# Performance work log

Hardware: AMD Instinct MI355X
Metric: run time of the kernel (lower is better)

## Reference

```python
import jax, jax.numpy as jnp
import numpy as np

B, S, D = 2, 2048, 2048
H = 16
HD = D // H  # 128
ROPE_BASE = 10000.0


def _rope_cos_sin(seq_len, head_dim):
    inv_freq = 1.0 / (ROPE_BASE ** (jnp.arange(0, head_dim, 2, dtype=jnp.float32) / head_dim))
    t = jnp.arange(seq_len, dtype=jnp.float32)
    freqs = jnp.einsum('i,j->ij', t, inv_freq)  # [S, HD/2]
    emb = jnp.concatenate([freqs, freqs], axis=-1)  # [S, HD]
    return jnp.cos(emb)[None, None], jnp.sin(emb)[None, None]  # [1,1,S,HD]


def _rotate_half(x):
    x1, x2 = jnp.split(x, 2, axis=-1)
    return jnp.concatenate([-x2, x1], axis=-1)


def setup_inputs() -> dict:
    key = jax.random.key(0)
    k1, k2, k3 = jax.random.split(key, 3)
    hidden_states = jax.random.normal(k1, (B, S, D), dtype=jnp.float32)
    w_qkv = jax.random.normal(k2, (D, 3 * D), dtype=jnp.float32) * (D ** -0.5)
    w_o = jax.random.normal(k3, (D, D), dtype=jnp.float32) * (D ** -0.5)
    return {"hidden_states": hidden_states, "w_qkv": w_qkv, "w_o": w_o}


def reference(hidden_states, w_qkv, w_o):
    b, s, _ = hidden_states.shape
    qkv = jnp.einsum('bsd,de->bse', hidden_states, w_qkv)  # [B,S,3D]
    q, k, v = jnp.split(qkv, 3, axis=-1)
    # [B,H,S,HD]
    q = q.reshape(b, s, H, HD).transpose(0, 2, 1, 3)
    k = k.reshape(b, s, H, HD).transpose(0, 2, 1, 3)
    v = v.reshape(b, s, H, HD).transpose(0, 2, 1, 3)
    cos, sin = _rope_cos_sin(s, HD)
    q = q * cos + _rotate_half(q) * sin
    k = k * cos + _rotate_half(k) * sin
    scale = 1.0 / np.sqrt(HD).astype(np.float32)
    scores = jnp.einsum('bhqd,bhkd->bhqk', q, k) * scale  # [B,H,S,S]
    causal = jnp.triu(jnp.ones((s, s), dtype=bool), k=1)
    scores = jnp.where(causal, -jnp.inf, scores)
    attn = jax.nn.softmax(scores, axis=-1)
    out = jnp.einsum('bhqk,bhkd->bhqd', attn, v)  # [B,H,S,HD]
    out = out.transpose(0, 2, 1, 3).reshape(b, s, H * HD)
    return jnp.einsum('bsd,de->bse', out, w_o)
```

## Files before the change

### kernel.cpp

```cpp
#include <hip/hip_runtime.h>
#include <math.h>

typedef unsigned short u16;
typedef short s16x8 __attribute__((ext_vector_type(8)));
typedef float f32x4 __attribute__((ext_vector_type(4)));

#define ATTN_SCALE 0.08838834764831845f
#define ATTN_SC2 0.1275174245f
#define NEG_BIG -1.0e30f

__device__ __forceinline__ u16 f2bf(float f) {
  union { float f; unsigned u; } c; c.f = f;
  return (u16)((c.u + 0x7fffu + ((c.u >> 16) & 1u)) >> 16);
}
__device__ __forceinline__ float bf2f(u16 v) {
  union { unsigned u; float f; } c; c.u = ((unsigned)v) << 16;
  return c.f;
}
__device__ __forceinline__ f32x4 mfma16(s16x8 a, s16x8 b, f32x4 c) {
  return __builtin_amdgcn_mfma_f32_16x16x32_bf16(a, b, c, 0, 0, 0);
}
__device__ __forceinline__ void gl_lds16(const u16* g, u16* l) {
  __builtin_amdgcn_global_load_lds(
      (const __attribute__((address_space(1))) unsigned int*)g,
      (__attribute__((address_space(3))) unsigned int*)l, 16, 0, 0);
}

__global__ __launch_bounds__(256) void k_cast(const float* __restrict__ in,
                                              u16* __restrict__ out, int n4) {
  const int i = blockIdx.x * 256 + threadIdx.x;
  if (i >= n4) return;
  const float4 v = ((const float4*)in)[i];
  ushort4 o;
  o.x = f2bf(v.x); o.y = f2bf(v.y); o.z = f2bf(v.z); o.w = f2bf(v.w);
  ((ushort4*)out)[i] = o;
}

__global__ __launch_bounds__(256) void k_transpose_cast(const float* __restrict__ in,
                                                        u16* __restrict__ out,
                                                        int R, int C) {
  __shared__ __attribute__((aligned(16))) u16 tile[32][33];
  const int c0 = blockIdx.x * 32, r0 = blockIdx.y * 32;
  const int tx = threadIdx.x, ty = threadIdx.y;
#pragma unroll
  for (int i = 0; i < 4; ++i)
    tile[ty + 8 * i][tx] = f2bf(in[(r0 + ty + 8 * i) * C + c0 + tx]);
  __syncthreads();
#pragma unroll
  for (int i = 0; i < 4; ++i)
    out[(c0 + ty + 8 * i) * R + r0 + tx] = tile[tx][ty + 8 * i];
}

__global__ __launch_bounds__(256) void k_vtrans(const u16* __restrict__ qkv,
                                                u16* __restrict__ vt) {
  __shared__ __attribute__((aligned(16))) u16 tile[32][33];
  const int bh = blockIdx.z, b = bh >> 4, h = bh & 15;
  const int s0 = blockIdx.x * 32, d0 = blockIdx.y * 32;
  const int tx = threadIdx.x, ty = threadIdx.y;
#pragma unroll
  for (int i = 0; i < 4; ++i) {
    const int s = s0 + ty + 8 * i;
    tile[ty + 8 * i][tx] = qkv[(b * 2048 + s) * 6144 + 4096 + h * 128 + d0 + tx];
  }
  __syncthreads();
#pragma unroll
  for (int i = 0; i < 4; ++i) {
    const int d = d0 + ty + 8 * i;
    vt[bh * 262144 + d * 2048 + s0 + tx] = tile[tx][ty + 8 * i];
  }
}

__global__ __launch_bounds__(256) void k_rope(u16* __restrict__ qkv) {
  const int id = blockIdx.x * 256 + threadIdx.x;
  const int j = id & 63;
  const int h = (id >> 6) & 15;
  const int sec = (id >> 10) & 1;
  const int m = id >> 11;
  const int s = m & 2047;
  const int base = m * 6144 + sec * 2048 + h * 128 + j;
  const float q0 = bf2f(qkv[base]);
  const float q1 = bf2f(qkv[base + 64]);
  const float inv = exp2f((float)j * -0.20762050593046014f);
  const float ang = (float)s * inv;
  float c, sn;
  sincosf(ang, &sn, &c);
  qkv[base]      = f2bf(q0 * c - q1 * sn);
  qkv[base + 64] = f2bf(q1 * c + q0 * sn);
}

template <bool A_F32, typename OUT_T>
__global__ __launch_bounds__(256) void k_gemm_lds(const void* __restrict__ Ap, int lda,
                                                  const u16* __restrict__ BT,
                                                  OUT_T* __restrict__ C, int ldc,
                                                  int K) {
  __shared__ __attribute__((aligned(16))) u16 As[128 * 32];
  __shared__ __attribute__((aligned(16))) u16 Bs[128 * 32];
  const int tid = threadIdx.x;
  const int lane = tid & 63, wave = tid >> 6;
  const int lm = lane & 15, quad = lane >> 4;
  const int wm = wave >> 1, wn = wave & 1;
  const int m0 = blockIdx.y * 128, n0 = blockIdx.x * 128;
  const int srow = lane >> 2, scol = (lane & 3) * 8;

  const f32x4 fzero = {0.f, 0.f, 0.f, 0.f};
  f32x4 acc[4][4];
#pragma unroll
  for (int i = 0; i < 4; ++i)
#pragma unroll
    for (int j = 0; j < 4; ++j) acc[i][j] = fzero;

  for (int k0 = 0; k0 < K; k0 += 32) {
    __syncthreads();
    if constexpr (A_F32) {
      const float* Af = (const float*)Ap;
#pragma unroll
      for (int i = 0; i < 2; ++i) {
        const int seg = tid + 256 * i;
        const int row = seg >> 2, c8 = (seg & 3) * 8;
        const float4 u = *(const float4*)&Af[(m0 + row) * lda + k0 + c8];
        const float4 w = *(const float4*)&Af[(m0 + row) * lda + k0 + c8 + 4];
        uint4 pk;
        pk.x = (unsigned)f2bf(u.x) | ((unsigned)f2bf(u.y) << 16);
        pk.y = (unsigned)f2bf(u.z) | ((unsigned)f2bf(u.w) << 16);
        pk.z = (unsigned)f2bf(w.x) | ((unsigned)f2bf(w.y) << 16);
        pk.w = (unsigned)f2bf(w.z) | ((unsigned)f2bf(w.w) << 16);
        *(uint4*)&As[row * 32 + c8] = pk;
      }
#pragma unroll
      for (int j = 0; j < 2; ++j) {
        const int rb = wave * 32 + j * 16;
        gl_lds16(&BT[(n0 + rb + srow) * K + k0 + scol], &Bs[rb * 32]);
      }
    } else {
      const u16* Ab = (const u16*)Ap;
#pragma unroll
      for (int j = 0; j < 2; ++j) {
        const int rb = wave * 32 + j * 16;
        gl_lds16(&Ab[(m0 + rb + srow) * lda + k0 + scol], &As[rb * 32]);
        gl_lds16(&BT[(n0 + rb + srow) * K + k0 + scol], &Bs[rb * 32]);
      }
    }
    __syncthreads();

    s16x8 af[4], bfr[4];
#pragma unroll
    for (int t = 0; t < 4; ++t) {
      af[t]  = *(const s16x8*)&As[(wm * 64 + t * 16 + lm) * 32 + quad * 8];
      bfr[t] = *(const s16x8*)&Bs[(wn * 64 + t * 16 + lm) * 32 + quad * 8];
    }
#pragma unroll
    for (int mt = 0; mt < 4; ++mt)
#pragma unroll
      for (int nt = 0; nt < 4; ++nt)
        acc[mt][nt] = mfma16(af[mt], bfr[nt], acc[mt][nt]);
  }
#pragma unroll
  for (int mt = 0; mt < 4; ++mt)
#pragma unroll
    for (int nt = 0; nt < 4; ++nt)
#pragma unroll
      for (int r = 0; r < 4; ++r) {
        const float v = acc[mt][nt][r];
        const int idx = (m0 + wm * 64 + mt * 16 + quad * 4 + r) * ldc +
                        n0 + wn * 64 + nt * 16 + lm;
        if constexpr (sizeof(OUT_T) == 2) C[idx] = f2bf(v);
        else                              C[idx] = v;
      }
}

template <typename OUT_T>
__global__ __launch_bounds__(512, 2) void k_gemm256(const u16* __restrict__ A, int lda,
                                                    const u16* __restrict__ BT, int ldb,
                                                    OUT_T* __restrict__ C, int ldc) {
  __shared__ __attribute__((aligned(16))) u16 As[3][2][256 * 32];
  __shared__ __attribute__((aligned(16))) u16 Bs[3][2][128 * 32];
  const int tid = threadIdx.x;
  const int lane = tid & 63, wave = tid >> 6;
  const int lm = lane & 15, quad = lane >> 4;
  const int wm = wave >> 1, wn = wave & 1;

  int bid = (blockIdx.x & 7) * (gridDim.x >> 3) + (blockIdx.x >> 3);
  const int m0 = (bid & 15) * 256;
  const int n0 = (bid >> 4) * 128;

  const int srow = lane >> 2, schunk = (lane & 3) * 8;
  auto stage_h = [&](int t, int h) {
    const int bi = t % 3;
    const int k0 = t * 64 + h * 32 + schunk;
    gl_lds16(&BT[(n0 + wave * 16 + srow) * ldb + k0],
             &Bs[bi][h][(wave * 16) * 32]);
    gl_lds16(&A[(m0 + wave * 32 + srow) * lda + k0],
             &As[bi][h][(wave * 32) * 32]);
    gl_lds16(&A[(m0 + wave * 32 + 16 + srow) * lda + k0],
             &As[bi][h][(wave * 32 + 16) * 32]);
  };

  const f32x4 fzero = {0.f, 0.f, 0.f, 0.f};
  f32x4 acc[4][4];
#pragma unroll
  for (int i = 0; i < 4; ++i)
#pragma unroll
    for (int j = 0; j < 4; ++j) acc[i][j] = fzero;

  stage_h(0, 0); stage_h(0, 1); stage_h(1, 0); stage_h(1, 1);
  asm volatile("s_waitcnt vmcnt(9)" ::: "memory");
  asm volatile("s_barrier" ::: "memory");

  for (int c = 0; c < 32; ++c) {
    const int bi = c % 3;
#pragma unroll
    for (int p = 0; p < 2; ++p) {
      s16x8 bfr[4], afr[4];
#pragma unroll
      for (int nt = 0; nt < 4; ++nt)
        bfr[nt] = *(const s16x8*)
            &Bs[bi][p][(wn * 64 + nt * 16 + lm) * 32 + quad * 8];
#pragma unroll
      for (int i = 0; i < 4; ++i)
        afr[i] = *(const s16x8*)
            &As[bi][p][(wm * 64 + i * 16 + lm) * 32 + quad * 8];
      if (c < 30) stage_h(c + 2, p);
      if (c < 30) {
        asm volatile("s_waitcnt vmcnt(9)" ::: "memory");
      } else if (c == 30) {
        if (p == 0) asm volatile("s_waitcnt vmcnt(6)" ::: "memory");
        else        asm volatile("s_waitcnt vmcnt(3)" ::: "memory");
      } else {
        if (p == 0) asm volatile("s_waitcnt vmcnt(0)" ::: "memory");
      }
      asm volatile("s_barrier" ::: "memory");
      __builtin_amdgcn_s_setprio(1);
#pragma unroll
      for (int i = 0; i < 4; ++i)
#pragma unroll
        for (int nt = 0; nt < 4; ++nt)
          acc[i][nt] = mfma16(afr[i], bfr[nt], acc[i][nt]);
      __builtin_amdgcn_s_setprio(0);
      if (!(c == 31 && p == 1)) asm volatile("s_barrier" ::: "memory");
    }
  }

#pragma unroll
  for (int i = 0; i < 4; ++i)
#pragma unroll
    for (int nt = 0; nt < 4; ++nt)
#pragma unroll
      for (int r = 0; r < 4; ++r) {
        const float v = acc[i][nt][r];
        const int idx = (m0 + wm * 64 + i * 16 + quad * 4 + r) * ldc +
                        n0 + wn * 64 + nt * 16 + lm;
        if constexpr (sizeof(OUT_T) == 2) C[idx] = f2bf(v);
        else                              C[idx] = v;
      }
}

__global__ __launch_bounds__(256) void k_attn(u16* __restrict__ qkv,
                                              const u16* __restrict__ vt) {
  __shared__ __attribute__((aligned(16))) u16 Ks[2][64 * 128];
  __shared__ __attribute__((aligned(16))) u16 Vs[2][128 * 64];
  __shared__ __attribute__((aligned(16))) u16 Ps[4 * 16 * 72];
  const int bh = blockIdx.x, pair = blockIdx.y;
  const int b = bh >> 4, h = bh & 15;
  const int tid = threadIdx.x;
  const int lane = tid & 63, wave = tid >> 6;
  const int lm = lane & 15, quad = lane >> 4;
  const int pbase = wave * 1152;
  const int sw = lm & 7;
  const f32x4 fzero = {0.f, 0.f, 0.f, 0.f};

  const int phase_end = pair;

  auto dma_tile = [&](int kt0, int buf) {
#pragma unroll
    for (int i = 0; i < 4; ++i) {
      const int row = i * 16 + wave * 4 + (lane >> 4);
      const int cc = (lane & 15) ^ (row & 7);
      gl_lds16(&qkv[(b * 2048 + kt0 + row) * 6144 + 2048 + h * 128 + cc * 8],
               &Ks[buf][(i * 16 + wave * 4) * 128]);
    }
#pragma unroll
    for (int i = 0; i < 4; ++i) {
      const int row = i * 32 + wave * 8 + (lane >> 3);
      const int cc = (lane & 7) ^ (row & 7);
      gl_lds16(&vt[bh * 262144 + row * 2048 + kt0 + cc * 8],
               &Vs[buf][(i * 32 + wave * 8) * 64]);
    }
  };

  dma_tile(0, 0);

  int qtile = pair;
  int qb = qtile * 64;
  int qrow = qb + wave * 16 + lm;
  int qoff = (b * 2048 + qrow) * 6144 + h * 128;
  s16x8 qfrag[4];
#pragma unroll
  for (int c = 0; c < 4; ++c)
    qfrag[c] = *(const s16x8*)&qkv[qoff + c * 32 + quad * 8];
  f32x4 o[8];
#pragma unroll
  for (int dt = 0; dt < 8; ++dt) o[dt] = fzero;
  float m_run = NEG_BIG, l_run = 0.f;

  __syncthreads();

  for (int it = 0; it < 33; ++it) {
    const int kt0 = (it <= phase_end ? it : it - phase_end - 1) * 64;
    const int buf = it & 1;

    if (it < 32) {
      const int nkt = (it + 1 <= phase_end ? it + 1 : it - phase_end) * 64;
      dma_tile(nkt, buf ^ 1);
    }

    f32x4 sa[4];
#pragma unroll
    for (int ss = 0; ss < 4; ++ss) sa[ss] = fzero;
#pragma unroll
    for (int ss = 0; ss < 4; ++ss)
#pragma unroll
      for (int c = 0; c < 4; ++c) {
        const int ccs = (c * 4 + quad) ^ sw;
        s16x8 a = *(const s16x8*)&Ks[buf][(ss * 16 + lm) * 128 + ccs * 8];
        sa[ss] = mfma16(a, qfrag[c], sa[ss]);
      }

    float p[4][4];
    float vmax = NEG_BIG;
    if (kt0 + 63 > qrow - lm) {
#pragma unroll
      for (int ss = 0; ss < 4; ++ss)
#pragma unroll
        for (int r = 0; r < 4; ++r) {
          const int kg = kt0 + ss * 16 + quad * 4 + r;
          float v = sa[ss][r] * ATTN_SC2;
          if (kg > qrow) v = NEG_BIG;
          p[ss][r] = v;
          vmax = fmaxf(vmax, v);
        }
    } else {
#pragma unroll
      for (int ss = 0; ss < 4; ++ss)
#pragma unroll
        for (int r = 0; r < 4; ++r) {
          const float v = sa[ss][r] * ATTN_SC2;
          p[ss][r] = v;
          vmax = fmaxf(vmax, v);
        }
    }
    vmax = fmaxf(vmax, __shfl_xor(vmax, 16, 64));
    vmax = fmaxf(vmax, __shfl_xor(vmax, 32, 64));
    if (!__all(vmax <= m_run)) {
      const float m_new = fmaxf(m_run, vmax);
      const float alpha = exp2f(m_run - m_new);
      l_run *= alpha;
#pragma unroll
      for (int dt = 0; dt < 8; ++dt) o[dt] *= alpha;
      m_run = m_new;
    }
    float rsum = 0.f;
#pragma unroll
    for (int ss = 0; ss < 4; ++ss)
#pragma unroll
      for (int r = 0; r < 4; ++r) {
        p[ss][r] = exp2f(p[ss][r] - m_run);
        rsum += p[ss][r];
      }
    rsum += __shfl_xor(rsum, 16, 64);
    rsum += __shfl_xor(rsum, 32, 64);
    l_run += rsum;

#pragma unroll
    for (int ss = 0; ss < 4; ++ss)
#pragma unroll
      for (int rp = 0; rp < 2; ++rp) {
        unsigned pk;
        asm("v_cvt_pk_bf16_f32 %0, %1, %2"
            : "=v"(pk) : "v"(p[ss][rp * 2]), "v"(p[ss][rp * 2 + 1]));
        *(unsigned*)&Ps[pbase + lm * 72 + ss * 16 + quad * 4 + rp * 2] = pk;
      }
    const s16x8 pv0 = *(const s16x8*)&Ps[pbase + lm * 72 + quad * 8];
    const s16x8 pv1 = *(const s16x8*)&Ps[pbase + lm * 72 + 32 + quad * 8];

#pragma unroll
    for (int dt = 0; dt < 8; ++dt) {
      const int c0 = (quad ^ sw) * 8, c1 = ((4 + quad) ^ sw) * 8;
      s16x8 a0 = *(const s16x8*)&Vs[buf][(dt * 16 + lm) * 64 + c0];
      s16x8 a1 = *(const s16x8*)&Vs[buf][(dt * 16 + lm) * 64 + c1];
      o[dt] = mfma16(a1, pv1, mfma16(a0, pv0, o[dt]));
    }

    if (it == phase_end) {
      const float inv_l = 1.0f / l_run;
#pragma unroll
      for (int dt = 0; dt < 8; ++dt)
#pragma unroll
        for (int r = 0; r < 4; ++r)
          qkv[qoff + dt * 16 + quad * 4 + r] = f2bf(o[dt][r] * inv_l);
      qtile = 31 - pair;
      qb = qtile * 64;
      qrow = qb + wave * 16 + lm;
      qoff = (b * 2048 + qrow) * 6144 + h * 128;
#pragma unroll
      for (int c = 0; c < 4; ++c)
        qfrag[c] = *(const s16x8*)&qkv[qoff + c * 32 + quad * 8];
#pragma unroll
      for (int dt = 0; dt < 8; ++dt) o[dt] = fzero;
      m_run = NEG_BIG; l_run = 0.f;
    }

    if (it < 32) __syncthreads();
  }

  const float inv_l = 1.0f / l_run;
#pragma unroll
  for (int dt = 0; dt < 8; ++dt)
#pragma unroll
    for (int r = 0; r < 4; ++r)
      qkv[qoff + dt * 16 + quad * 4 + r] = f2bf(o[dt][r] * inv_l);
}

extern "C" void kernel_launch(void* const* d_in, const int* in_sizes, int n_in,
                              void* d_out, int out_size, void* d_ws, size_t ws_size,
                              hipStream_t stream) {
  const float* hidden = (const float*)d_in[0];
  const float* w_qkv  = (const float*)d_in[1];
  const float* w_o    = (const float*)d_in[2];
  float* out = (float*)d_out;
  u16* ws = (u16*)d_ws;

  u16* qkv   = ws;
  u16* wqkvT = ws + 25165824;
  u16* vt    = ws + 25165824;
  u16* woT   = ws + 33554432;
  u16* hb    = ws + 37748736;
  const bool fast = ws_size >= (size_t)46137344 * 2;

  dim3 tb(32, 8);
  k_transpose_cast<<<dim3(192, 64), tb, 0, stream>>>(w_qkv, wqkvT, 2048, 6144);
  if (fast) {
    k_cast<<<8192, 256, 0, stream>>>(hidden, hb, 2097152);
    k_gemm256<u16><<<768, 512, 0, stream>>>(hb, 2048, wqkvT, 2048, qkv, 6144);
  } else {
    k_gemm_lds<true, u16><<<dim3(48, 32), 256, 0, stream>>>(hidden, 2048, wqkvT,
                                                            qkv, 6144, 2048);
  }
  k_rope<<<32768, 256, 0, stream>>>(qkv);
  k_vtrans<<<dim3(64, 4, 32), tb, 0, stream>>>(qkv, vt);
  k_transpose_cast<<<dim3(64, 64), tb, 0, stream>>>(w_o, woT, 2048, 2048);
  k_attn<<<dim3(32, 16), 256, 0, stream>>>(qkv, vt);
  if (fast) {
    k_gemm256<float><<<256, 512, 0, stream>>>(qkv, 6144, woT, 2048, out, 2048);
  } else {
    k_gemm_lds<false, float><<<dim3(16, 32), 256, 0, stream>>>(qkv, 6144, woT,
                                                               out, 2048, 2048);
  }
}
```

Before: 410.1 us.

## Process two 16-row query groups per wave to reuse K/V fragments

Each wave now handles 32 query rows (two groups of 16) instead of 16, so the block's query tile grows from 64 to 128 rows. K and V fragments are loaded from LDS once per tile and fed to MFMAs for both groups, which halves LDS reads per unit of compute and halves the number of blocks and K/V tile streams. The paired causal schedule is adjusted to 128-row tiles and launch_bounds(256,1) is set. In exchange register pressure rises considerably and the grid shrinks to 256 blocks, which lowers occupancy and parallelism.

After: 432.5 us. 1.05x slower.

```diff
diff --git a/kernel.cpp b/kernel.cpp
--- a/kernel.cpp
+++ b/kernel.cpp
@@ -254,8 +254,8 @@
       }
 }
 
-__global__ __launch_bounds__(256) void k_attn(u16* __restrict__ qkv,
-                                              const u16* __restrict__ vt) {
+__global__ __launch_bounds__(256, 1) void k_attn(u16* __restrict__ qkv,
+                                                 const u16* __restrict__ vt) {
   __shared__ __attribute__((aligned(16))) u16 Ks[2][64 * 128];
   __shared__ __attribute__((aligned(16))) u16 Vs[2][128 * 64];
   __shared__ __attribute__((aligned(16))) u16 Ps[4 * 16 * 72];
@@ -268,7 +268,7 @@
   const int sw = lm & 7;
   const f32x4 fzero = {0.f, 0.f, 0.f, 0.f};
 
-  const int phase_end = pair;
+  const int phase_end = 2 * pair + 1;
 
   auto dma_tile = [&](int kt0, int buf) {
 #pragma unroll
@@ -289,135 +289,164 @@
 
   dma_tile(0, 0);
 
+  int qbase[2], qoff[2];
+  s16x8 qfrag[2][4];
   int qtile = pair;
-  int qb = qtile * 64;
-  int qrow = qb + wave * 16 + lm;
-  int qoff = (b * 2048 + qrow) * 6144 + h * 128;
-  s16x8 qfrag[4];
-#pragma unroll
-  for (int c = 0; c < 4; ++c)
-    qfrag[c] = *(const s16x8*)&qkv[qoff + c * 32 + quad * 8];
-  f32x4 o[8];
-#pragma unroll
-  for (int dt = 0; dt < 8; ++dt) o[dt] = fzero;
-  float m_run = NEG_BIG, l_run = 0.f;
+#pragma unroll
+  for (int g = 0; g < 2; ++g) {
+    qbase[g] = qtile * 128 + wave * 32 + g * 16;
+    qoff[g] = (b * 2048 + qbase[g] + lm) * 6144 + h * 128;
+#pragma unroll
+    for (int c = 0; c < 4; ++c)
+      qfrag[g][c] = *(const s16x8*)&qkv[qoff[g] + c * 32 + quad * 8];
+  }
+  f32x4 o[2][8];
+#pragma unroll
+  for (int g = 0; g < 2; ++g)
+#pragma unroll
+    for (int dt = 0; dt < 8; ++dt) o[g][dt] = fzero;
+  float mrun[2] = {NEG_BIG, NEG_BIG}, lrun[2] = {0.f, 0.f};
 
   __syncthreads();
 
-  for (int it = 0; it < 33; ++it) {
+  for (int it = 0; it < 34; ++it) {
     const int kt0 = (it <= phase_end ? it : it - phase_end - 1) * 64;
     const int buf = it & 1;
 
-    if (it < 32) {
+    if (it < 33) {
       const int nkt = (it + 1 <= phase_end ? it + 1 : it - phase_end) * 64;
       dma_tile(nkt, buf ^ 1);
     }
 
-    f32x4 sa[4];
-#pragma unroll
-    for (int ss = 0; ss < 4; ++ss) sa[ss] = fzero;
+    s16x8 tf[16];
 #pragma unroll
     for (int ss = 0; ss < 4; ++ss)
 #pragma unroll
       for (int c = 0; c < 4; ++c) {
         const int ccs = (c * 4 + quad) ^ sw;
-        s16x8 a = *(const s16x8*)&Ks[buf][(ss * 16 + lm) * 128 + ccs * 8];
-        sa[ss] = mfma16(a, qfrag[c], sa[ss]);
-      }
-
-    float p[4][4];
-    float vmax = NEG_BIG;
-    if (kt0 + 63 > qrow - lm) {
+        tf[ss * 4 + c] = *(const s16x8*)&Ks[buf][(ss * 16 + lm) * 128 + ccs * 8];
+      }
+
+    s16x8 pv[2][2];
+#pragma unroll
+    for (int g = 0; g < 2; ++g) {
+      f32x4 sa[4];
+#pragma unroll
+      for (int ss = 0; ss < 4; ++ss) sa[ss] = fzero;
 #pragma unroll
       for (int ss = 0; ss < 4; ++ss)
 #pragma unroll
+        for (int c = 0; c < 4; ++c)
+          sa[ss] = mfma16(tf[ss * 4 + c], qfrag[g][c], sa[ss]);
+
+      const int qrow = qbase[g] + lm;
+      float p[4][4];
+      float vmax = NEG_BIG;
+      if (kt0 + 63 > qbase[g]) {
+#pragma unroll
+        for (int ss = 0; ss < 4; ++ss)
+#pragma unroll
+          for (int r = 0; r < 4; ++r) {
+            const int kg = kt0 + ss * 16 + quad * 4 + r;
+            float v = sa[ss][r] * ATTN_SC2;
+            if (kg > qrow) v = NEG_BIG;
+            p[ss][r] = v;
+            vmax = fmaxf(vmax, v);
+          }
+      } else {
+#pragma unroll
+        for (int ss = 0; ss < 4; ++ss)
+#pragma unroll
+          for (int r = 0; r < 4; ++r) {
+            const float v = sa[ss][r] * ATTN_SC2;
+            p[ss][r] = v;
+            vmax = fmaxf(vmax, v);
+          }
+      }
+      vmax = fmaxf(vmax, __shfl_xor(vmax, 16, 64));
+      vmax = fmaxf(vmax, __shfl_xor(vmax, 32, 64));
+      if (!__all(vmax <= mrun[g])) {
+        const float m_new = fmaxf(mrun[g], vmax);
+        const float alpha = exp2f(mrun[g] - m_new);
+        lrun[g] *= alpha;
+#pragma unroll
+        for (int dt = 0; dt < 8; ++dt) o[g][dt] *= alpha;
+        mrun[g] = m_new;
+      }
+      float rsum = 0.f;
+#pragma unroll
+      for (int ss = 0; ss < 4; ++ss)
+#pragma unroll
         for (int r = 0; r < 4; ++r) {
-          const int kg = kt0 + ss * 16 + quad * 4 + r;
-          float v = sa[ss][r] * ATTN_SC2;
-          if (kg > qrow) v = NEG_BIG;
-          p[ss][r] = v;
-          vmax = fmaxf(vmax, v);
+          p[ss][r] = exp2f(p[ss][r] - mrun[g]);
+          rsum += p[ss][r];
         }
-    } else {
+      rsum += __shfl_xor(rsum, 16, 64);
+      rsum += __shfl_xor(rsum, 32, 64);
+      lrun[g] += rsum;
+
 #pragma unroll
       for (int ss = 0; ss < 4; ++ss)
 #pragma unroll
-        for (int r = 0; r < 4; ++r) {
-          const float v = sa[ss][r] * ATTN_SC2;
-          p[ss][r] = v;
-          vmax = fmaxf(vmax, v);
+        for (int rp = 0; rp < 2; ++rp) {
+          unsigned pk;
+          asm("v_cvt_pk_bf16_f32 %0, %1, %2"
+              : "=v"(pk) : "v"(p[ss][rp * 2]), "v"(p[ss][rp * 2 + 1]));
+          *(unsigned*)&Ps[pbase + lm * 72 + ss * 16 + quad * 4 + rp * 2] = pk;
         }
-    }
-    vmax = fmaxf(vmax, __shfl_xor(vmax, 16, 64));
-    vmax = fmaxf(vmax, __shfl_xor(vmax, 32, 64));
-    if (!__all(vmax <= m_run)) {
-      const float m_new = fmaxf(m_run, vmax);
-      const float alpha = exp2f(m_run - m_new);
-      l_run *= alpha;
-#pragma unroll
-      for (int dt = 0; dt < 8; ++dt) o[dt] *= alpha;
-      m_run = m_new;
-    }
-    float rsum = 0.f;
-#pragma unroll
-    for (int ss = 0; ss < 4; ++ss)
-#pragma unroll
-      for (int r = 0; r < 4; ++r) {
-        p[ss][r] = exp2f(p[ss][r] - m_run);
-        rsum += p[ss][r];
-      }
-    rsum += __shfl_xor(rsum, 16, 64);
-    rsum += __shfl_xor(rsum, 32, 64);
-    l_run += rsum;
-
-#pragma unroll
-    for (int ss = 0; ss < 4; ++ss)
-#pragma unroll
-      for (int rp = 0; rp < 2; ++rp) {
-        unsigned pk;
-        asm("v_cvt_pk_bf16_f32 %0, %1, %2"
-            : "=v"(pk) : "v"(p[ss][rp * 2]), "v"(p[ss][rp * 2 + 1]));
-        *(unsigned*)&Ps[pbase + lm * 72 + ss * 16 + quad * 4 + rp * 2] = pk;
-      }
-    const s16x8 pv0 = *(const s16x8*)&Ps[pbase + lm * 72 + quad * 8];
-    const s16x8 pv1 = *(const s16x8*)&Ps[pbase + lm * 72 + 32 + quad * 8];
+      pv[g][0] = *(const s16x8*)&Ps[pbase + lm * 72 + quad * 8];
+      pv[g][1] = *(const s16x8*)&Ps[pbase + lm * 72 + 32 + quad * 8];
+    }
 
 #pragma unroll
     for (int dt = 0; dt < 8; ++dt) {
       const int c0 = (quad ^ sw) * 8, c1 = ((4 + quad) ^ sw) * 8;
-      s16x8 a0 = *(const s16x8*)&Vs[buf][(dt * 16 + lm) * 64 + c0];
-      s16x8 a1 = *(const s16x8*)&Vs[buf][(dt * 16 + lm) * 64 + c1];
-      o[dt] = mfma16(a1, pv1, mfma16(a0, pv0, o[dt]));
-    }
+      tf[dt * 2]     = *(const s16x8*)&Vs[buf][(dt * 16 + lm) * 64 + c0];
+      tf[dt * 2 + 1] = *(const s16x8*)&Vs[buf][(dt * 16 + lm) * 64 + c1];
+    }
+#pragma unroll
+    for (int g = 0; g < 2; ++g)
+#pragma unroll
+      for (int dt = 0; dt < 8; ++dt)
+        o[g][dt] = mfma16(tf[dt * 2 + 1], pv[g][1],
+                          mfma16(tf[dt * 2], pv[g][0], o[g][dt]));
 
     if (it == phase_end) {
-      const float inv_l = 1.0f / l_run;
-#pragma unroll
-      for (int dt = 0; dt < 8; ++dt)
-#pragma unroll
-        for (int r = 0; r < 4; ++r)
-          qkv[qoff + dt * 16 + quad * 4 + r] = f2bf(o[dt][r] * inv_l);
-      qtile = 31 - pair;
-      qb = qtile * 64;
-      qrow = qb + wave * 16 + lm;
-      qoff = (b * 2048 + qrow) * 6144 + h * 128;
-#pragma unroll
-      for (int c = 0; c < 4; ++c)
-        qfrag[c] = *(const s16x8*)&qkv[qoff + c * 32 + quad * 8];
-#pragma unroll
-      for (int dt = 0; dt < 8; ++dt) o[dt] = fzero;
-      m_run = NEG_BIG; l_run = 0.f;
-    }
-
-    if (it < 32) __syncthreads();
-  }
-
-  const float inv_l = 1.0f / l_run;
-#pragma unroll
-  for (int dt = 0; dt < 8; ++dt)
-#pragma unroll
-    for (int r = 0; r < 4; ++r)
-      qkv[qoff + dt * 16 + quad * 4 + r] = f2bf(o[dt][r] * inv_l);
+#pragma unroll
+      for (int g = 0; g < 2; ++g) {
+        const float inv_l = 1.0f / lrun[g];
+#pragma unroll
+        for (int dt = 0; dt < 8; ++dt)
+#pragma unroll
+          for (int r = 0; r < 4; ++r)
+            qkv[qoff[g] + dt * 16 + quad * 4 + r] = f2bf(o[g][dt][r] * inv_l);
+      }
+      qtile = 15 - pair;
+#pragma unroll
+      for (int g = 0; g < 2; ++g) {
+        qbase[g] = qtile * 128 + wave * 32 + g * 16;
+        qoff[g] = (b * 2048 + qbase[g] + lm) * 6144 + h * 128;
+#pragma unroll
+        for (int c = 0; c < 4; ++c)
+          qfrag[g][c] = *(const s16x8*)&qkv[qoff[g] + c * 32 + quad * 8];
+#pragma unroll
+        for (int dt = 0; dt < 8; ++dt) o[g][dt] = fzero;
+        mrun[g] = NEG_BIG; lrun[g] = 0.f;
+      }
+    }
+
+    if (it < 33) __syncthreads();
+  }
+
+#pragma unroll
+  for (int g = 0; g < 2; ++g) {
+    const float inv_l = 1.0f / lrun[g];
+#pragma unroll
+    for (int dt = 0; dt < 8; ++dt)
+#pragma unroll
+      for (int r = 0; r < 4; ++r)
+        qkv[qoff[g] + dt * 16 + quad * 4 + r] = f2bf(o[g][dt][r] * inv_l);
+  }
 }
 
 extern "C" void kernel_launch(void* const* d_in, const int* in_sizes, int n_in,
@@ -448,7 +477,7 @@
   k_rope<<<32768, 256, 0, stream>>>(qkv);
   k_vtrans<<<dim3(64, 4, 32), tb, 0, stream>>>(qkv, vt);
   k_transpose_cast<<<dim3(64, 64), tb, 0, stream>>>(w_o, woT, 2048, 2048);
-  k_attn<<<dim3(32, 16), 256, 0, stream>>>(qkv, vt);
+  k_attn<<<dim3(32, 8), 256, 0, stream>>>(qkv, vt);
   if (fast) {
     k_gemm256<float><<<256, 512, 0, stream>>>(qkv, 6144, woT, 2048, out, 2048);
   } else {
```

## Fuse RoPE into QKV GEMM epilogue via LDS partner exchange

Applied to the files above, without the earlier changes.

Applies rotary embedding directly in the QKV GEMM epilogue for the Q and K column tiles and drops the separate k_rope launch on the fast path. Each wave writes its accumulators to shared memory, which is aliased over the staging buffers. It then reads the partner wave's values for the rotated half and computes sin and cos per element before storing bf16. This removes a full read-modify-write pass over the Q and K activations and one launch, at the cost of an extra barrier-synchronised LDS exchange and per-element transcendental work in the epilogue.

New measurement: 484.0 us. 18.0% more time.

```diff
diff --git a/kernel.cpp b/kernel.cpp
--- a/kernel.cpp
+++ b/kernel.cpp
@@ -168,12 +168,11 @@
       }
 }
 
-template <typename OUT_T>
+template <typename OUT_T, bool ROPE>
 __global__ __launch_bounds__(512, 2) void k_gemm256(const u16* __restrict__ A, int lda,
                                                     const u16* __restrict__ BT, int ldb,
                                                     OUT_T* __restrict__ C, int ldc) {
-  __shared__ __attribute__((aligned(16))) u16 As[3][2][256 * 32];
-  __shared__ __attribute__((aligned(16))) u16 Bs[3][2][128 * 32];
+  __shared__ __attribute__((aligned(16))) u16 S[73728];
   const int tid = threadIdx.x;
   const int lane = tid & 63, wave = tid >> 6;
   const int lm = lane & 15, quad = lane >> 4;
@@ -184,15 +183,17 @@
   const int n0 = (bid >> 4) * 128;
 
   const int srow = lane >> 2, schunk = (lane & 3) * 8;
+  auto As_p = [&](int bi, int h) -> u16* { return &S[bi * 16384 + h * 8192]; };
+  auto Bs_p = [&](int bi, int h) -> u16* { return &S[49152 + bi * 8192 + h * 4096]; };
   auto stage_h = [&](int t, int h) {
     const int bi = t % 3;
     const int k0 = t * 64 + h * 32 + schunk;
     gl_lds16(&BT[(n0 + wave * 16 + srow) * ldb + k0],
-             &Bs[bi][h][(wave * 16) * 32]);
+             Bs_p(bi, h) + (wave * 16) * 32);
     gl_lds16(&A[(m0 + wave * 32 + srow) * lda + k0],
-             &As[bi][h][(wave * 32) * 32]);
+             As_p(bi, h) + (wave * 32) * 32);
     gl_lds16(&A[(m0 + wave * 32 + 16 + srow) * lda + k0],
-             &As[bi][h][(wave * 32 + 16) * 32]);
+             As_p(bi, h) + (wave * 32 + 16) * 32);
   };
 
   const f32x4 fzero = {0.f, 0.f, 0.f, 0.f};
@@ -214,11 +215,11 @@
 #pragma unroll
       for (int nt = 0; nt < 4; ++nt)
         bfr[nt] = *(const s16x8*)
-            &Bs[bi][p][(wn * 64 + nt * 16 + lm) * 32 + quad * 8];
+            &Bs_p(bi, p)[(wn * 64 + nt * 16 + lm) * 32 + quad * 8];
 #pragma unroll
       for (int i = 0; i < 4; ++i)
         afr[i] = *(const s16x8*)
-            &As[bi][p][(wm * 64 + i * 16 + lm) * 32 + quad * 8];
+            &As_p(bi, p)[(wm * 64 + i * 16 + lm) * 32 + quad * 8];
       if (c < 30) stage_h(c + 2, p);
       if (c < 30) {
         asm volatile("s_waitcnt vmcnt(9)" ::: "memory");
@@ -240,18 +241,59 @@
     }
   }
 
-#pragma unroll
-  for (int i = 0; i < 4; ++i)
-#pragma unroll
-    for (int nt = 0; nt < 4; ++nt)
-#pragma unroll
-      for (int r = 0; r < 4; ++r) {
-        const float v = acc[i][nt][r];
-        const int idx = (m0 + wm * 64 + i * 16 + quad * 4 + r) * ldc +
-                        n0 + wn * 64 + nt * 16 + lm;
-        if constexpr (sizeof(OUT_T) == 2) C[idx] = f2bf(v);
-        else                              C[idx] = v;
-      }
+  if (ROPE && n0 < 4096) {
+    __syncthreads();
+    float2* Ex = (float2*)S;
+#pragma unroll
+    for (int i = 0; i < 4; ++i)
+#pragma unroll
+      for (int nt = 0; nt < 4; ++nt)
+#pragma unroll
+        for (int rp = 0; rp < 2; ++rp) {
+          float2 v;
+          v.x = acc[i][nt][rp * 2];
+          v.y = acc[i][nt][rp * 2 + 1];
+          Ex[((i * 8 + nt * 2 + rp) * 8 + wave) * 64 + lane] = v;
+        }
+    __syncthreads();
+    const float sgn = (wn == 0) ? -1.f : 1.f;
+#pragma unroll
+    for (int nt = 0; nt < 4; ++nt) {
+      const int j = nt * 16 + lm;
+      const float inv = exp2f((float)j * -0.20762050593046014f);
+#pragma unroll
+      for (int i = 0; i < 4; ++i)
+#pragma unroll
+        for (int rp = 0; rp < 2; ++rp) {
+          const float2 par = Ex[((i * 8 + nt * 2 + rp) * 8 + (wave ^ 1)) * 64 + lane];
+#pragma unroll
+          for (int q2 = 0; q2 < 2; ++q2) {
+            const int r = rp * 2 + q2;
+            const int gr = m0 + wm * 64 + i * 16 + quad * 4 + r;
+            const float ang = (float)(gr & 2047) * inv;
+            float cc, sn;
+            sincosf(ang, &sn, &cc);
+            const float own = acc[i][nt][r];
+            const float p1 = (q2 == 0) ? par.x : par.y;
+            ((u16*)C)[gr * ldc + n0 + wn * 64 + nt * 16 + lm] =
+                f2bf(own * cc + sgn * p1 * sn);
+          }
+        }
+    }
+  } else {
+#pragma unroll
+    for (int i = 0; i < 4; ++i)
+#pragma unroll
+      for (int nt = 0; nt < 4; ++nt)
+#pragma unroll
+        for (int r = 0; r < 4; ++r) {
+          const float v = acc[i][nt][r];
+          const int idx = (m0 + wm * 64 + i * 16 + quad * 4 + r) * ldc +
+                          n0 + wn * 64 + nt * 16 + lm;
+          if constexpr (sizeof(OUT_T) == 2) C[idx] = f2bf(v);
+          else                              C[idx] = v;
+        }
+  }
 }
 
 __global__ __launch_bounds__(256) void k_attn(u16* __restrict__ qkv,
@@ -440,17 +482,19 @@
   k_transpose_cast<<<dim3(192, 64), tb, 0, stream>>>(w_qkv, wqkvT, 2048, 6144);
   if (fast) {
     k_cast<<<8192, 256, 0, stream>>>(hidden, hb, 2097152);
-    k_gemm256<u16><<<768, 512, 0, stream>>>(hb, 2048, wqkvT, 2048, qkv, 6144);
+    k_gemm256<u16, true><<<768, 512, 0, stream>>>(hb, 2048, wqkvT, 2048,
+                                                  qkv, 6144);
   } else {
     k_gemm_lds<true, u16><<<dim3(48, 32), 256, 0, stream>>>(hidden, 2048, wqkvT,
                                                             qkv, 6144, 2048);
-  }
-  k_rope<<<32768, 256, 0, stream>>>(qkv);
+    k_rope<<<32768, 256, 0, stream>>>(qkv);
+  }
   k_vtrans<<<dim3(64, 4, 32), tb, 0, stream>>>(qkv, vt);
   k_transpose_cast<<<dim3(64, 64), tb, 0, stream>>>(w_o, woT, 2048, 2048);
   k_attn<<<dim3(32, 16), 256, 0, stream>>>(qkv, vt);
   if (fast) {
-    k_gemm256<float><<<256, 512, 0, stream>>>(qkv, 6144, woT, 2048, out, 2048);
+    k_gemm256<float, false><<<256, 512, 0, stream>>>(qkv, 6144, woT, 2048,
+                                                     out, 2048);
   } else {
     k_gemm_lds<false, float><<<dim3(16, 32), 256, 0, stream>>>(qkv, 6144, woT,
                                                                out, 2048, 2048);
```
